# Performance work log

Hardware: AMD Instinct MI355X
Metric: run time of the kernel (lower is better)

The kernel has to match this reference:

```python
import jax, jax.numpy as jnp
import numpy as np

N_NODES = 22
K_NEIGHBOR = 4
BN_EPS = 1e-5


def _conv1d(x, w):
    # x: (B, C, L), w: (O, C, 7), stride 1, padding 3
    return jax.lax.conv_general_dilated(x, w, (1,), [(3, 3)],
                                        dimension_numbers=('NCH', 'OIH', 'NCH'))


def _block(x, w, gamma, beta):
    # x: (N, B, C, L) -> conv + per-node BatchNorm (train-mode batch stats,
    # matching the original per-node loop) + ReLU + MaxPool1d(2)
    n, b, c, l = x.shape
    y = _conv1d(x.reshape(n * b, c, l), w)            # (N*B, O, L)
    o, lo = y.shape[1], y.shape[2]
    y = y.reshape(n, b, o, lo)
    mean = y.mean(axis=(1, 3), keepdims=True)
    var = y.var(axis=(1, 3), keepdims=True)
    y = (y - mean) * jax.lax.rsqrt(var + BN_EPS)
    y = y * gamma[None, None, :, None] + beta[None, None, :, None]
    y = jax.nn.relu(y)
    y = y.reshape(n, b, o, lo // 2, 2).max(axis=-1)   # MaxPool1d(2)
    return y


def _adj_matrix(feat, k):
    # feat: (B, N, D). Squared euclidean distances, k nearest (incl. self), row-normalized.
    sq = jnp.sum(feat ** 2, axis=2, keepdims=True)            # (B, N, 1)
    dist = sq + jnp.swapaxes(sq, 1, 2) - 2.0 * jnp.einsum('bnd,bmd->bnm', feat, feat)
    _, idx = jax.lax.top_k(-dist, k)                          # smallest-k indices, (B, N, k)
    adj = jax.nn.one_hot(idx, feat.shape[1], dtype=feat.dtype).sum(axis=2)
    return adj * (1.0 / k)


def setup_inputs() -> dict:
    key = jax.random.key(0)
    ks = jax.random.split(key, 20)
    B, N, T = 256, N_NODES, 2000
    f32 = jnp.float32
    inp = {
        'x': jax.random.normal(ks[0], (B, N, T), f32),
        # conv stack (shared across all electrode nodes)
        'w1': jax.random.normal(ks[1], (4, 1, 7), f32) * 0.2,
        'g1': jnp.ones((4,), f32), 'b1': jnp.zeros((4,), f32),
        'w2': jax.random.normal(ks[2], (8, 4, 7), f32) * 0.1,
        'g2': jnp.ones((8,), f32), 'b2': jnp.zeros((8,), f32),
        'w3': jax.random.normal(ks[3], (16, 8, 7), f32) * 0.1,
        'g3': jnp.ones((16,), f32), 'b3': jnp.zeros((16,), f32),
        # graph convolutions (uniform init like torch module)
        'gw1': jax.random.uniform(ks[4], (16, 32), f32, -1/np.sqrt(32), 1/np.sqrt(32)),
        'gb1': jax.random.uniform(ks[5], (1, 1, 32), f32, -1/np.sqrt(32), 1/np.sqrt(32)),
        'gw2': jax.random.uniform(ks[6], (32, 64), f32, -1/np.sqrt(64), 1/np.sqrt(64)),
        'gb2': jax.random.uniform(ks[7], (1, 1, 64), f32, -1/np.sqrt(64), 1/np.sqrt(64)),
        'gw3': jax.random.uniform(ks[8], (64, 128), f32, -1/np.sqrt(128), 1/np.sqrt(128)),
        'gb3': jax.random.uniform(ks[9], (1, 1, 128), f32, -1/np.sqrt(128), 1/np.sqrt(128)),
        # heads (stored as (in, out))
        'fw1': jax.random.normal(ks[10], (128, 64), f32) * 0.05,
        'fb1': jnp.zeros((64,), f32),
        'fw2': jax.random.normal(ks[11], (64, 4), f32) * 0.05,
        'fb2': jnp.zeros((4,), f32),
    }
    return inp


def reference(x, w1, g1, b1, w2, g2, b2, w3, g3, b3,
              gw1, gb1, gw2, gb2, gw3, gb3, fw1, fb1, fw2, fb2):
    B, N, T = x.shape
    # --- MultiChannelConv (vectorized over electrode nodes) ---
    h = jnp.transpose(x, (1, 0, 2))[:, :, None, :]   # (N, B, 1, T)
    h = _block(h, w1, g1, b1)                        # (N, B, 4, T/2)
    h = _block(h, w2, g2, b2)                        # (N, B, 8, T/4)
    h = _block(h, w3, g3, b3)                        # (N, B, 16, T/8)
    feat = h.mean(axis=-1)                           # AdaptiveAvgPool1d(1) -> (N, B, 16)
    feat = jnp.transpose(feat, (1, 0, 2))            # (B, N, 16)
    # --- adjacency from top-k nearest neighbors ---
    adj = _adj_matrix(feat, K_NEIGHBOR)              # (B, N, N)
    # --- graph convolutions ---
    x1 = jax.nn.relu(jnp.einsum('bnm,bmf->bnf', adj, feat @ gw1) + gb1)
    x2 = jax.nn.relu(jnp.einsum('bnm,bmf->bnf', adj, x1 @ gw2) + gb2)
    x3 = jax.nn.relu(jnp.einsum('bnm,bmf->bnf', adj, x2 @ gw3) + gb3)
    # mean over nodes, then MLP head
    pooled = x3.mean(axis=1)                         # (B, 128)
    out = (pooled @ fw1 + fb1) @ fw2 + fb2           # (B, nclass)
    return out
```

## Files before the change

### kernel.cpp

```cpp
#include <hip/hip_runtime.h>

#define BSZ 256
#define NND 22
#define BN_EPS 1e-5f

typedef float v2f __attribute__((ext_vector_type(2)));

__device__ __forceinline__ v2f pkfma(v2f a, v2f b, v2f c) {
  return __builtin_elementwise_fma(a, b, c);
}

template<int CIN, int COUT, int R, int SROW>
__device__ __forceinline__ void conv_coreR(
    const float (*s_in)[SROW], const float* s_w, int tid, float y[COUT][R]) {
#pragma unroll
  for (int o = 0; o < COUT; o++)
#pragma unroll
    for (int r = 0; r < R; r++) y[o][r] = 0.f;
#pragma unroll 1
  for (int c = 0; c < CIN; c++) {
    float xr[R + 6];
    const float4* xp = (const float4*)&s_in[c][4 * tid];
    float4 xa = xp[0], xb = xp[1];
    float2 xc = *(const float2*)&s_in[c][4 * tid + 8];
    xr[0] = xa.x; xr[1] = xa.y; xr[2] = xa.z; xr[3] = xa.w;
    xr[4] = xb.x; xr[5] = xb.y; xr[6] = xb.z; xr[7] = xb.w;
    xr[8] = xc.x; xr[9] = xc.y;
#pragma unroll
    for (int k = 0; k < 7; k++) {
      const float4* wp = (const float4*)&s_w[(c * 7 + k) * COUT];
#pragma unroll
      for (int o4 = 0; o4 < COUT / 4; o4++) {
        float4 wv = wp[o4];
#pragma unroll
        for (int r = 0; r < R; r++) {
          y[4 * o4 + 0][r] += wv.x * xr[r + k];
          y[4 * o4 + 1][r] += wv.y * xr[r + k];
          y[4 * o4 + 2][r] += wv.z * xr[r + k];
          y[4 * o4 + 3][r] += wv.w * xr[r + k];
        }
      }
    }
  }
}

template<int CIN, int COUT, int NTH>
__device__ __forceinline__ void stage_weights(const float* __restrict__ w,
                                              float* s_w, int tid) {
  for (int i = tid; i < CIN * 7 * COUT; i += NTH) {
    int c = i / (7 * COUT), k = (i / COUT) % 7, o = i % COUT;
    s_w[i] = w[(o * CIN + c) * 7 + k];
  }
}

template<int CIN, int COUT, int LIN, int NTH, int NT, int R>
__global__ __launch_bounds__(NTH) void conv_stats1p(
    const float* __restrict__ in, long sn, long sb, long sc,
    const float* __restrict__ w, float* __restrict__ part,
    float* __restrict__ y1p) {
  const int TILE = R * NTH;
  const int SROW = TILE + 8;
  __shared__ alignas(16) float s_in[CIN][SROW];
  __shared__ alignas(16) float s_w[CIN * 7 * COUT];
  __shared__ float s_red[2][NTH / 64][COUT];
  int tid = threadIdx.x, n = blockIdx.z, b = blockIdx.y;
  int t0 = blockIdx.x * TILE;
  const float* base = in + (long)n * sn + (long)b * sb;
  stage_weights<CIN, COUT, NTH>(w, s_w, tid);
  for (int c = 0; c < CIN; c++)
    for (int i = tid; i < TILE + 6; i += NTH) {
      int l = t0 + i - 3;
      s_in[c][i] = (l >= 0 && l < LIN) ? base[(long)c * sc + l] : 0.f;
    }
  __syncthreads();
  float y[COUT][R];
  conv_coreR<CIN, COUT, R, SROW>(s_in, s_w, tid, y);
  bool valid = (t0 + R * tid) < LIN;
  if (valid) {
    int p0 = (t0 + R * tid) >> 1;
    long yb = ((long)n * BSZ + b) * 4000 + p0;
#pragma unroll
    for (int o = 0; o < COUT; o++) {
      float2 v;
      v.x = fmaxf(y[o][0], y[o][1]);
      v.y = fmaxf(y[o][2], y[o][3]);
      *(float2*)&y1p[yb + (long)o * 1000] = v;
    }
  }
  int lane = tid & 63, wv = tid >> 6;
#pragma unroll
  for (int o = 0; o < COUT; o++) {
    float s = 0.f, q = 0.f;
    if (valid) {
#pragma unroll
      for (int r = 0; r < R; r++) { s += y[o][r]; q += y[o][r] * y[o][r]; }
    }
#pragma unroll
    for (int off = 32; off > 0; off >>= 1) {
      s += __shfl_down(s, off, 64);
      q += __shfl_down(q, off, 64);
    }
    if (lane == 0) { s_red[0][wv][o] = s; s_red[1][wv][o] = q; }
  }
  __syncthreads();
  if (tid < COUT) {
    float s = 0.f, q = 0.f;
#pragma unroll
    for (int g = 0; g < NTH / 64; g++) { s += s_red[0][g][tid]; q += s_red[1][g][tid]; }
    long slot = ((long)n * NT + blockIdx.x) * BSZ + b;
    part[slot * (2 * COUT) + tid] = s;
    part[slot * (2 * COUT) + COUT + tid] = q;
  }
}

template<int C, int NSLOT, int LIN>
__global__ __launch_bounds__(256) void stats_reduce(
    const float* __restrict__ part,
    const float* __restrict__ gamma, const float* __restrict__ beta,
    float* __restrict__ scs,
    const float* __restrict__ w2, const float* __restrict__ w3,
    float* __restrict__ w2t, float* __restrict__ w3t) {
  const int V = 2 * C;
  const int GRP = 256 / V;
  int n = blockIdx.x, tid = threadIdx.x;
  int j = tid % V, g = tid / V;
  const float* p = part + (long)n * NSLOT * V;
  float s = 0.f;
  for (int sl = g; sl < NSLOT; sl += GRP) s += p[(long)sl * V + j];
  __shared__ float red[V][GRP];
  __shared__ float tot[V];
  red[j][g] = s;
  __syncthreads();
  if (tid < V) {
    float t = 0.f;
#pragma unroll
    for (int gg = 0; gg < GRP; gg++) t += red[tid][gg];
    tot[tid] = t;
  }
  __syncthreads();
  if (tid < C) {
    float cnt = (float)BSZ * (float)LIN;
    float m = tot[tid] / cnt;
    float var = tot[C + tid] / cnt - m * m;
    float istd = 1.0f / sqrtf(var + BN_EPS);
    float scl = gamma[tid] * istd;
    scs[n * 64 + tid] = scl;
    scs[n * 64 + 32 + tid] = beta[tid] - m * scl;
  }
  if (w2t != nullptr && blockIdx.x == 0) {
    if (tid < 224) {
      int c = tid / 56, k = (tid / 8) % 7, o = tid & 7;
      w2t[tid] = w2[(o * 4 + c) * 7 + k];
    }
    for (int i = tid; i < 896; i += 256) {
      int c = i / 112, k = (i / 16) % 7, o = i & 15;
      w3t[i] = w3[(o * 8 + c) * 7 + k];
    }
  }
}

__global__ __launch_bounds__(256) void fused1(
    const float* __restrict__ y1p,
    const float* __restrict__ scs1,
    const float* __restrict__ w2t,
    float* __restrict__ y2p,
    float* __restrict__ p2) {
  __shared__ alignas(16) float s_w2[224];
  __shared__ float s_red[2][4][8];
  int tid = threadIdx.x, n = blockIdx.z, b = blockIdx.y;
  if (tid < 224) s_w2[tid] = w2t[tid];
  __syncthreads();
  bool valid = tid < 250;
  v2f y2v[4][4];
#pragma unroll
  for (int oo = 0; oo < 4; oo++)
#pragma unroll
    for (int r = 0; r < 4; r++) { y2v[oo][r].x = 0.f; y2v[oo][r].y = 0.f; }
  if (valid) {
    const float* yrow = y1p + ((long)n * BSZ + b) * 4000;
    bool p0 = (tid == 0), pE = (tid == 249);
    int offA = p0 ? 0 : 4 * tid - 4;
    int offB = 4 * tid;
    int offC = pE ? 996 : 4 * tid + 4;
    float4 nA = *(const float4*)&yrow[offA];
    float4 nB = *(const float4*)&yrow[offB];
    float4 nC = *(const float4*)&yrow[offC];
#pragma unroll 1
    for (int c = 0; c < 4; c++) {
      float4 A = nA, B = nB, C = nC;
      const float* nxt = yrow + (c + 1) * 1000;
      nA = *(const float4*)&nxt[offA];
      nB = *(const float4*)&nxt[offB];
      nC = *(const float4*)&nxt[offC];
      float sc = scs1[n * 64 + c], sh = scs1[n * 64 + 32 + c];
      float xr[12];
      xr[0] = A.x; xr[1] = A.y; xr[2] = A.z; xr[3] = A.w;
      xr[4] = B.x; xr[5] = B.y; xr[6] = B.z; xr[7] = B.w;
      xr[8] = C.x; xr[9] = C.y; xr[10] = C.z; xr[11] = C.w;
#pragma unroll
      for (int j = 0; j < 12; j++) xr[j] = fmaxf(xr[j] * sc + sh, 0.f);
      if (p0) { xr[1] = 0.f; xr[2] = 0.f; xr[3] = 0.f; }
      if (pE) { xr[8] = 0.f; xr[9] = 0.f; xr[10] = 0.f; }
#pragma unroll
      for (int k = 0; k < 7; k++) {
        float4 w0 = *(const float4*)&s_w2[(c * 7 + k) * 8];
        float4 w1v = *(const float4*)&s_w2[(c * 7 + k) * 8 + 4];
        v2f wp0, wp1, wp2, wp3;
        wp0.x = w0.x; wp0.y = w0.y;
        wp1.x = w0.z; wp1.y = w0.w;
        wp2.x = w1v.x; wp2.y = w1v.y;
        wp3.x = w1v.z; wp3.y = w1v.w;
#pragma unroll
        for (int r = 0; r < 4; r++) {
          v2f xs; xs.x = xr[r + k + 1]; xs.y = xr[r + k + 1];
          y2v[0][r] = pkfma(wp0, xs, y2v[0][r]);
          y2v[1][r] = pkfma(wp1, xs, y2v[1][r]);
          y2v[2][r] = pkfma(wp2, xs, y2v[2][r]);
          y2v[3][r] = pkfma(wp3, xs, y2v[3][r]);
        }
      }
    }
    long yb = ((long)n * BSZ + b) * 4000 + 2 * tid;
#pragma unroll
    for (int oo = 0; oo < 4; oo++) {
      float2 vx, vy;
      vx.x = fmaxf(y2v[oo][0].x, y2v[oo][1].x);
      vx.y = fmaxf(y2v[oo][2].x, y2v[oo][3].x);
      *(float2*)&y2p[yb + (2 * oo) * 500] = vx;
      vy.x = fmaxf(y2v[oo][0].y, y2v[oo][1].y);
      vy.y = fmaxf(y2v[oo][2].y, y2v[oo][3].y);
      *(float2*)&y2p[yb + (2 * oo + 1) * 500] = vy;
    }
  }
  int lane = tid & 63, wv = tid >> 6;
#pragma unroll
  for (int o = 0; o < 8; o++) {
    float g0 = (o & 1) ? y2v[o >> 1][0].y : y2v[o >> 1][0].x;
    float g1 = (o & 1) ? y2v[o >> 1][1].y : y2v[o >> 1][1].x;
    float g2 = (o & 1) ? y2v[o >> 1][2].y : y2v[o >> 1][2].x;
    float g3 = (o & 1) ? y2v[o >> 1][3].y : y2v[o >> 1][3].x;
    float s = g0 + g1 + g2 + g3;
    float q = g0 * g0 + g1 * g1 + g2 * g2 + g3 * g3;
#pragma unroll
    for (int off = 32; off > 0; off >>= 1) {
      s += __shfl_down(s, off, 64);
      q += __shfl_down(q, off, 64);
    }
    if (lane == 0) { s_red[0][wv][o] = s; s_red[1][wv][o] = q; }
  }
  __syncthreads();
  if (tid < 8) {
    float s = 0.f, q = 0.f;
#pragma unroll
    for (int g = 0; g < 4; g++) { s += s_red[0][g][tid]; q += s_red[1][g][tid]; }
    long slot = (long)n * BSZ + b;
    p2[slot * 16 + tid] = s;
    p2[slot * 16 + 8 + tid] = q;
  }
}

__global__ __launch_bounds__(256) void fused2(
    const float* __restrict__ y2p,
    const float* __restrict__ scs2,
    const float* __restrict__ w3t,
    float* __restrict__ y3p,
    float* __restrict__ p3) {
  __shared__ alignas(16) float s_w3[896];
  __shared__ float s_red[2][4][8];
  int tid = threadIdx.x, n = blockIdx.z, b = blockIdx.y;
  for (int i = tid; i < 896; i += 256) s_w3[i] = w3t[i];
  __syncthreads();
  int og = __builtin_amdgcn_readfirstlane(tid >> 7);
  int pt = tid & 127;
  bool valid = pt < 125;
  v2f y3v[4][4];
#pragma unroll
  for (int oo = 0; oo < 4; oo++)
#pragma unroll
    for (int r = 0; r < 4; r++) { y3v[oo][r].x = 0.f; y3v[oo][r].y = 0.f; }
  if (valid) {
    const float* yrow = y2p + ((long)n * BSZ + b) * 4000;
    bool p0 = (pt == 0), pE = (pt == 124);
    int offA = p0 ? 0 : 4 * pt - 4;
    int offB = 4 * pt;
    int offC = pE ? 496 : 4 * pt + 4;
    float4 nA = *(const float4*)&yrow[offA];
    float4 nB = *(const float4*)&yrow[offB];
    float4 nC = *(const float4*)&yrow[offC];
#pragma unroll 1
    for (int c = 0; c < 8; c++) {
      float4 A = nA, B = nB, C = nC;
      const float* nxt = yrow + (c + 1) * 500;
      nA = *(const float4*)&nxt[offA];
      nB = *(const float4*)&nxt[offB];
      nC = *(const float4*)&nxt[offC];
      float sc = scs2[n * 64 + c], sh = scs2[n * 64 + 32 + c];
      float xr[12];
      xr[0] = A.x; xr[1] = A.y; xr[2] = A.z; xr[3] = A.w;
      xr[4] = B.x; xr[5] = B.y; xr[6] = B.z; xr[7] = B.w;
      xr[8] = C.x; xr[9] = C.y; xr[10] = C.z; xr[11] = C.w;
#pragma unroll
      for (int j = 0; j < 12; j++) xr[j] = fmaxf(xr[j] * sc + sh, 0.f);
      if (p0) { xr[1] = 0.f; xr[2] = 0.f; xr[3] = 0.f; }
      if (pE) { xr[8] = 0.f; xr[9] = 0.f; xr[10] = 0.f; }
#pragma unroll
      for (int k = 0; k < 7; k++) {
        float4 w0 = *(const float4*)&s_w3[(c * 7 + k) * 16 + og * 8];
        float4 w1v = *(const float4*)&s_w3[(c * 7 + k) * 16 + og * 8 + 4];
        v2f wp0, wp1, wp2, wp3;
        wp0.x = w0.x; wp0.y = w0.y;
        wp1.x = w0.z; wp1.y = w0.w;
        wp2.x = w1v.x; wp2.y = w1v.y;
        wp3.x = w1v.z; wp3.y = w1v.w;
#pragma unroll
        for (int r = 0; r < 4; r++) {
          v2f xs; xs.x = xr[r + k + 1]; xs.y = xr[r + k + 1];
          y3v[0][r] = pkfma(wp0, xs, y3v[0][r]);
          y3v[1][r] = pkfma(wp1, xs, y3v[1][r]);
          y3v[2][r] = pkfma(wp2, xs, y3v[2][r]);
          y3v[3][r] = pkfma(wp3, xs, y3v[3][r]);
        }
      }
    }
    long yb = (((long)n * BSZ + b) * 16 + og * 8) * 250 + 2 * pt;
#pragma unroll
    for (int oo = 0; oo < 4; oo++) {
      float2 vx, vy;
      vx.x = fmaxf(y3v[oo][0].x, y3v[oo][1].x);
      vx.y = fmaxf(y3v[oo][2].x, y3v[oo][3].x);
      *(float2*)&y3p[yb + (2 * oo) * 250] = vx;
      vy.x = fmaxf(y3v[oo][0].y, y3v[oo][1].y);
      vy.y = fmaxf(y3v[oo][2].y, y3v[oo][3].y);
      *(float2*)&y3p[yb + (2 * oo + 1) * 250] = vy;
    }
  }
  int lane = tid & 63, wv = tid >> 6;
#pragma unroll
  for (int o = 0; o < 8; o++) {
    float g0 = (o & 1) ? y3v[o >> 1][0].y : y3v[o >> 1][0].x;
    float g1 = (o & 1) ? y3v[o >> 1][1].y : y3v[o >> 1][1].x;
    float g2 = (o & 1) ? y3v[o >> 1][2].y : y3v[o >> 1][2].x;
    float g3 = (o & 1) ? y3v[o >> 1][3].y : y3v[o >> 1][3].x;
    float s = g0 + g1 + g2 + g3;
    float q = g0 * g0 + g1 * g1 + g2 * g2 + g3 * g3;
#pragma unroll
    for (int off = 32; off > 0; off >>= 1) {
      s += __shfl_down(s, off, 64);
      q += __shfl_down(q, off, 64);
    }
    if (lane == 0) { s_red[0][wv][o] = s; s_red[1][wv][o] = q; }
  }
  __syncthreads();
  if (tid < 16) {
    int og2 = tid >> 3, o = tid & 7;
    float s = s_red[0][2 * og2][o] + s_red[0][2 * og2 + 1][o];
    float q = s_red[1][2 * og2][o] + s_red[1][2 * og2 + 1][o];
    long slot = (long)n * BSZ + b;
    p3[slot * 32 + tid] = s;
    p3[slot * 32 + 16 + tid] = q;
  }
}

__global__ __launch_bounds__(256) void feat_apply(
    const float* __restrict__ y3p,
    const float* __restrict__ scs3,
    float* __restrict__ feat) {
  int tid = threadIdx.x, n = blockIdx.z, b = blockIdx.y;
  int ch = tid >> 4, s = tid & 15;
  const float* yb = y3p + (((long)n * BSZ + b) * 16 + ch) * 250;
  float sc = scs3[n * 64 + ch], sh = scs3[n * 64 + 32 + ch];
  float acc = 0.f;
  for (int j = s; j < 125; j += 16) {
    float2 v = *(const float2*)&yb[2 * j];
    acc += fmaxf(v.x * sc + sh, 0.f) + fmaxf(v.y * sc + sh, 0.f);
  }
#pragma unroll
  for (int off = 8; off > 0; off >>= 1) acc += __shfl_down(acc, off, 16);
  if (s == 0) feat[((long)b * NND + n) * 16 + ch] = acc * (1.0f / 250.f);
}

__global__ __launch_bounds__(256) void graph_head(
    const float* __restrict__ feat,
    const float* __restrict__ gw1, const float* __restrict__ gb1,
    const float* __restrict__ gw2, const float* __restrict__ gb2,
    const float* __restrict__ gw3, const float* __restrict__ gb3,
    const float* __restrict__ fw1, const float* __restrict__ fb1,
    const float* __restrict__ fw2, const float* __restrict__ fb2,
    float* __restrict__ out) {
  int b = blockIdx.x, tid = threadIdx.x;
  __shared__ float s_feat[NND][16];
  __shared__ float s_sq[NND];
  __shared__ float s_dist[NND][NND];
  __shared__ float s_adj[NND][NND];
  __shared__ float s_x[NND][128];
  __shared__ float s_t[NND][128];
  __shared__ float s_pool[128];
  __shared__ float s_h[64];
  for (int i = tid; i < NND * 16; i += 256) s_feat[i >> 4][i & 15] = feat[b * NND * 16 + i];
  __syncthreads();
  if (tid < NND) {
    float s = 0.f;
    for (int c = 0; c < 16; c++) s += s_feat[tid][c] * s_feat[tid][c];
    s_sq[tid] = s;
  }
  __syncthreads();
  for (int i = tid; i < NND * NND; i += 256) {
    int nn = i / NND, m = i % NND;
    float d = 0.f;
    for (int c = 0; c < 16; c++) d += s_feat[nn][c] * s_feat[m][c];
    s_dist[nn][m] = s_sq[nn] + s_sq[m] - 2.f * d;
    s_adj[nn][m] = 0.f;
  }
  __syncthreads();
  if (tid < NND) {
    unsigned used = 0;
    for (int j = 0; j < 4; j++) {
      float best = 3.4e38f; int bi = 0;
      for (int m = 0; m < NND; m++)
        if (!((used >> m) & 1u) && s_dist[tid][m] < best) { best = s_dist[tid][m]; bi = m; }
      used |= 1u << bi;
      s_adj[tid][bi] = 0.25f;
    }
  }
  __syncthreads();
  for (int i = tid; i < NND * 32; i += 256) {
    int nn = i / 32, f = i % 32;
    float a = 0.f;
    for (int c = 0; c < 16; c++) a += s_feat[nn][c] * gw1[c * 32 + f];
    s_t[nn][f] = a;
  }
  __syncthreads();
  for (int i = tid; i < NND * 32; i += 256) {
    int nn = i / 32, f = i % 32;
    float a = gb1[f];
    for (int m = 0; m < NND; m++) a += s_adj[nn][m] * s_t[m][f];
    s_x[nn][f] = fmaxf(a, 0.f);
  }
  __syncthreads();
  for (int i = tid; i < NND * 64; i += 256) {
    int nn = i / 64, f = i % 64;
    float a = 0.f;
    for (int c = 0; c < 32; c++) a += s_x[nn][c] * gw2[c * 64 + f];
    s_t[nn][f] = a;
  }
  __syncthreads();
  for (int i = tid; i < NND * 64; i += 256) {
    int nn = i / 64, f = i % 64;
    float a = gb2[f];
    for (int m = 0; m < NND; m++) a += s_adj[nn][m] * s_t[m][f];
    s_x[nn][f] = fmaxf(a, 0.f);
  }
  __syncthreads();
  for (int i = tid; i < NND * 128; i += 256) {
    int nn = i / 128, f = i % 128;
    float a = 0.f;
    for (int c = 0; c < 64; c++) a += s_x[nn][c] * gw3[c * 128 + f];
    s_t[nn][f] = a;
  }
  __syncthreads();
  for (int i = tid; i < NND * 128; i += 256) {
    int nn = i / 128, f = i % 128;
    float a = gb3[f];
    for (int m = 0; m < NND; m++) a += s_adj[nn][m] * s_t[m][f];
    s_x[nn][f] = fmaxf(a, 0.f);
  }
  __syncthreads();
  if (tid < 128) {
    float a = 0.f;
    for (int m = 0; m < NND; m++) a += s_x[m][tid];
    s_pool[tid] = a * (1.0f / (float)NND);
  }
  __syncthreads();
  if (tid < 64) {
    float a = fb1[tid];
    for (int c = 0; c < 128; c++) a += s_pool[c] * fw1[c * 64 + tid];
    s_h[tid] = a;
  }
  __syncthreads();
  if (tid < 4) {
    float a = fb2[tid];
    for (int c = 0; c < 64; c++) a += s_h[c] * fw2[c * 4 + tid];
    out[b * 4 + tid] = a;
  }
}

extern "C" void kernel_launch(void* const* d_in, const int* in_sizes, int n_in,
                              void* d_out, int out_size, void* d_ws, size_t ws_size,
                              hipStream_t stream) {
  (void)in_sizes; (void)n_in; (void)out_size; (void)ws_size;
  const float* x   = (const float*)d_in[0];
  const float* w1  = (const float*)d_in[1];
  const float* g1  = (const float*)d_in[2];
  const float* b1  = (const float*)d_in[3];
  const float* w2  = (const float*)d_in[4];
  const float* g2  = (const float*)d_in[5];
  const float* b2  = (const float*)d_in[6];
  const float* w3  = (const float*)d_in[7];
  const float* g3  = (const float*)d_in[8];
  const float* b3  = (const float*)d_in[9];
  const float* gw1 = (const float*)d_in[10];
  const float* gb1 = (const float*)d_in[11];
  const float* gw2 = (const float*)d_in[12];
  const float* gb2 = (const float*)d_in[13];
  const float* gw3 = (const float*)d_in[14];
  const float* gb3 = (const float*)d_in[15];
  const float* fw1 = (const float*)d_in[16];
  const float* fb1 = (const float*)d_in[17];
  const float* fw2 = (const float*)d_in[18];
  const float* fb2 = (const float*)d_in[19];

  float* ws = (float*)d_ws;
  const long RSZ = (long)NND * BSZ * 4000;
  float* y1p  = ws;
  float* y3p  = ws;
  float* y2p  = ws + RSZ;
  float* feat = y2p + RSZ;
  float* scs1 = feat + (long)BSZ * NND * 16;
  float* scs2 = scs1 + NND * 64;
  float* scs3 = scs2 + NND * 64;
  float* p1   = scs3 + NND * 64;
  float* p2   = p1 + (long)NND * 512 * 8;
  float* p3   = p2 + (long)NND * 256 * 16;
  float* w2t  = p3 + (long)NND * 256 * 32;
  float* w3t  = w2t + 224;

  conv_stats1p<1, 4, 2000, 256, 2, 4><<<dim3(2, BSZ, NND), dim3(256), 0, stream>>>(
      x, 2000, (long)NND * 2000, 0, w1, p1, y1p);
  stats_reduce<4, 512, 2000><<<dim3(NND), dim3(256), 0, stream>>>(
      p1, g1, b1, scs1, w2, w3, w2t, w3t);
  fused1<<<dim3(1, BSZ, NND), dim3(256), 0, stream>>>(y1p, scs1, w2t, y2p, p2);
  stats_reduce<8, 256, 1000><<<dim3(NND), dim3(256), 0, stream>>>(
      p2, g2, b2, scs2, nullptr, nullptr, nullptr, nullptr);
  fused2<<<dim3(1, BSZ, NND), dim3(256), 0, stream>>>(y2p, scs2, w3t, y3p, p3);
  stats_reduce<16, 256, 500><<<dim3(NND), dim3(256), 0, stream>>>(
      p3, g3, b3, scs3, nullptr, nullptr, nullptr, nullptr);
  feat_apply<<<dim3(1, BSZ, NND), dim3(256), 0, stream>>>(y3p, scs3, feat);
  graph_head<<<dim3(BSZ), dim3(256), 0, stream>>>(
      feat, gw1, gb1, gw2, gb2, gw3, gb3, fw1, fb1, fw2, fb2, (float*)d_out);
}
```

Measured before the change: 212.3 us.

## Compute all 16 conv3 channels per thread and read weights directly from global

```diff
diff --git a/kernel.cpp b/kernel.cpp
--- a/kernel.cpp
+++ b/kernel.cpp
@@ -165,11 +165,8 @@
     const float* __restrict__ w2t,
     float* __restrict__ y2p,
     float* __restrict__ p2) {
-  __shared__ alignas(16) float s_w2[224];
   __shared__ float s_red[2][4][8];
   int tid = threadIdx.x, n = blockIdx.z, b = blockIdx.y;
-  if (tid < 224) s_w2[tid] = w2t[tid];
-  __syncthreads();
   bool valid = tid < 250;
   v2f y2v[4][4];
 #pragma unroll
@@ -203,8 +200,8 @@
       if (pE) { xr[8] = 0.f; xr[9] = 0.f; xr[10] = 0.f; }
 #pragma unroll
       for (int k = 0; k < 7; k++) {
-        float4 w0 = *(const float4*)&s_w2[(c * 7 + k) * 8];
-        float4 w1v = *(const float4*)&s_w2[(c * 7 + k) * 8 + 4];
+        float4 w0 = *(const float4*)&w2t[(c * 7 + k) * 8];
+        float4 w1v = *(const float4*)&w2t[(c * 7 + k) * 8 + 4];
         v2f wp0, wp1, wp2, wp3;
         wp0.x = w0.x; wp0.y = w0.y;
         wp1.x = w0.z; wp1.y = w0.w;
@@ -259,31 +256,26 @@
   }
 }
 
-__global__ __launch_bounds__(256) void fused2(
+__global__ __launch_bounds__(128) void fused2(
     const float* __restrict__ y2p,
     const float* __restrict__ scs2,
     const float* __restrict__ w3t,
     float* __restrict__ y3p,
     float* __restrict__ p3) {
-  __shared__ alignas(16) float s_w3[896];
-  __shared__ float s_red[2][4][8];
+  __shared__ float s_red[2][2][16];
   int tid = threadIdx.x, n = blockIdx.z, b = blockIdx.y;
-  for (int i = tid; i < 896; i += 256) s_w3[i] = w3t[i];
-  __syncthreads();
-  int og = __builtin_amdgcn_readfirstlane(tid >> 7);
-  int pt = tid & 127;
-  bool valid = pt < 125;
-  v2f y3v[4][4];
-#pragma unroll
-  for (int oo = 0; oo < 4; oo++)
-#pragma unroll
-    for (int r = 0; r < 4; r++) { y3v[oo][r].x = 0.f; y3v[oo][r].y = 0.f; }
+  bool valid = tid < 125;
+  v2f acc[8][4];
+#pragma unroll
+  for (int oo = 0; oo < 8; oo++)
+#pragma unroll
+    for (int r = 0; r < 4; r++) { acc[oo][r].x = 0.f; acc[oo][r].y = 0.f; }
   if (valid) {
     const float* yrow = y2p + ((long)n * BSZ + b) * 4000;
-    bool p0 = (pt == 0), pE = (pt == 124);
-    int offA = p0 ? 0 : 4 * pt - 4;
-    int offB = 4 * pt;
-    int offC = pE ? 496 : 4 * pt + 4;
+    bool p0 = (tid == 0), pE = (tid == 124);
+    int offA = p0 ? 0 : 4 * tid - 4;
+    int offB = 4 * tid;
+    int offC = pE ? 496 : 4 * tid + 4;
     float4 nA = *(const float4*)&yrow[offA];
     float4 nB = *(const float4*)&yrow[offB];
     float4 nC = *(const float4*)&yrow[offC];
@@ -305,42 +297,49 @@
       if (pE) { xr[8] = 0.f; xr[9] = 0.f; xr[10] = 0.f; }
 #pragma unroll
       for (int k = 0; k < 7; k++) {
-        float4 w0 = *(const float4*)&s_w3[(c * 7 + k) * 16 + og * 8];
-        float4 w1v = *(const float4*)&s_w3[(c * 7 + k) * 16 + og * 8 + 4];
-        v2f wp0, wp1, wp2, wp3;
-        wp0.x = w0.x; wp0.y = w0.y;
-        wp1.x = w0.z; wp1.y = w0.w;
-        wp2.x = w1v.x; wp2.y = w1v.y;
-        wp3.x = w1v.z; wp3.y = w1v.w;
+        const float* wb = &w3t[(c * 7 + k) * 16];
+        float4 w0 = *(const float4*)&wb[0];
+        float4 w1v = *(const float4*)&wb[4];
+        float4 w2v = *(const float4*)&wb[8];
+        float4 w3v = *(const float4*)&wb[12];
+        v2f wp0, wp1, wp2, wp3, wp4, wp5, wp6, wp7;
+        wp0.x = w0.x; wp0.y = w0.y;   wp1.x = w0.z; wp1.y = w0.w;
+        wp2.x = w1v.x; wp2.y = w1v.y; wp3.x = w1v.z; wp3.y = w1v.w;
+        wp4.x = w2v.x; wp4.y = w2v.y; wp5.x = w2v.z; wp5.y = w2v.w;
+        wp6.x = w3v.x; wp6.y = w3v.y; wp7.x = w3v.z; wp7.y = w3v.w;
 #pragma unroll
         for (int r = 0; r < 4; r++) {
           v2f xs; xs.x = xr[r + k + 1]; xs.y = xr[r + k + 1];
-          y3v[0][r] = pkfma(wp0, xs, y3v[0][r]);
-          y3v[1][r] = pkfma(wp1, xs, y3v[1][r]);
-          y3v[2][r] = pkfma(wp2, xs, y3v[2][r]);
-          y3v[3][r] = pkfma(wp3, xs, y3v[3][r]);
+          acc[0][r] = pkfma(wp0, xs, acc[0][r]);
+          acc[1][r] = pkfma(wp1, xs, acc[1][r]);
+          acc[2][r] = pkfma(wp2, xs, acc[2][r]);
+          acc[3][r] = pkfma(wp3, xs, acc[3][r]);
+          acc[4][r] = pkfma(wp4, xs, acc[4][r]);
+          acc[5][r] = pkfma(wp5, xs, acc[5][r]);
+          acc[6][r] = pkfma(wp6, xs, acc[6][r]);
+          acc[7][r] = pkfma(wp7, xs, acc[7][r]);
         }
       }
     }
-    long yb = (((long)n * BSZ + b) * 16 + og * 8) * 250 + 2 * pt;
-#pragma unroll
-    for (int oo = 0; oo < 4; oo++) {
+    long yb = ((long)n * BSZ + b) * 4000 + 2 * tid;
+#pragma unroll
+    for (int oo = 0; oo < 8; oo++) {
       float2 vx, vy;
-      vx.x = fmaxf(y3v[oo][0].x, y3v[oo][1].x);
-      vx.y = fmaxf(y3v[oo][2].x, y3v[oo][3].x);
+      vx.x = fmaxf(acc[oo][0].x, acc[oo][1].x);
+      vx.y = fmaxf(acc[oo][2].x, acc[oo][3].x);
       *(float2*)&y3p[yb + (2 * oo) * 250] = vx;
-      vy.x = fmaxf(y3v[oo][0].y, y3v[oo][1].y);
-      vy.y = fmaxf(y3v[oo][2].y, y3v[oo][3].y);
+      vy.x = fmaxf(acc[oo][0].y, acc[oo][1].y);
+      vy.y = fmaxf(acc[oo][2].y, acc[oo][3].y);
       *(float2*)&y3p[yb + (2 * oo + 1) * 250] = vy;
     }
   }
   int lane = tid & 63, wv = tid >> 6;
 #pragma unroll
-  for (int o = 0; o < 8; o++) {
-    float g0 = (o & 1) ? y3v[o >> 1][0].y : y3v[o >> 1][0].x;
-    float g1 = (o & 1) ? y3v[o >> 1][1].y : y3v[o >> 1][1].x;
-    float g2 = (o & 1) ? y3v[o >> 1][2].y : y3v[o >> 1][2].x;
-    float g3 = (o & 1) ? y3v[o >> 1][3].y : y3v[o >> 1][3].x;
+  for (int o = 0; o < 16; o++) {
+    float g0 = (o & 1) ? acc[o >> 1][0].y : acc[o >> 1][0].x;
+    float g1 = (o & 1) ? acc[o >> 1][1].y : acc[o >> 1][1].x;
+    float g2 = (o & 1) ? acc[o >> 1][2].y : acc[o >> 1][2].x;
+    float g3 = (o & 1) ? acc[o >> 1][3].y : acc[o >> 1][3].x;
     float s = g0 + g1 + g2 + g3;
     float q = g0 * g0 + g1 * g1 + g2 * g2 + g3 * g3;
 #pragma unroll
@@ -352,9 +351,8 @@
   }
   __syncthreads();
   if (tid < 16) {
-    int og2 = tid >> 3, o = tid & 7;
-    float s = s_red[0][2 * og2][o] + s_red[0][2 * og2 + 1][o];
-    float q = s_red[1][2 * og2][o] + s_red[1][2 * og2 + 1][o];
+    float s = s_red[0][0][tid] + s_red[0][1][tid];
+    float q = s_red[1][0][tid] + s_red[1][1][tid];
     long slot = (long)n * BSZ + b;
     p3[slot * 32 + tid] = s;
     p3[slot * 32 + 16 + tid] = q;
@@ -531,7 +529,7 @@
   fused1<<<dim3(1, BSZ, NND), dim3(256), 0, stream>>>(y1p, scs1, w2t, y2p, p2);
   stats_reduce<8, 256, 1000><<<dim3(NND), dim3(256), 0, stream>>>(
       p2, g2, b2, scs2, nullptr, nullptr, nullptr, nullptr);
-  fused2<<<dim3(1, BSZ, NND), dim3(256), 0, stream>>>(y2p, scs2, w3t, y3p, p3);
+  fused2<<<dim3(1, BSZ, NND), dim3(128), 0, stream>>>(y2p, scs2, w3t, y3p, p3);
   stats_reduce<16, 256, 500><<<dim3(NND), dim3(256), 0, stream>>>(
       p3, g3, b3, scs3, nullptr, nullptr, nullptr, nullptr);
   feat_apply<<<dim3(1, BSZ, NND), dim3(256), 0, stream>>>(y3p, scs3, feat);
```

New measurement: 199.7 us (median of 2 runs). 5.9% less time.
